# Kernel optimization log

Hardware: AMD Instinct MI355X
Metric: run time of the kernel (lower is better)

The kernel has to match this reference:

```python
import jax, jax.numpy as jnp
import numpy as np

IN_DIM = 64  # channels; theta/phi -> C//8, g -> C//2


def _maxpool2x2(t):
    # t: [B, c, H, W] -> [B, c, H//2, W//2]
    B, c, H, W = t.shape
    return t.reshape(B, c, H // 2, 2, W // 2, 2).max(axis=(3, 5))


def setup_inputs() -> dict:
    key = jax.random.key(0)
    ks = jax.random.split(key, 6)
    C = IN_DIM
    x = jax.random.normal(ks[0], (16, C, 64, 64), dtype=jnp.float32)
    # 1x1 convs stored as [out, in] matrices (kernel is 1x1, no bias)
    w_theta = jax.random.normal(ks[1], (C // 8, C), dtype=jnp.float32) * (1.0 / np.sqrt(C))
    w_phi = jax.random.normal(ks[2], (C // 8, C), dtype=jnp.float32) * (1.0 / np.sqrt(C))
    w_g = jax.random.normal(ks[3], (C // 2, C), dtype=jnp.float32) * (1.0 / np.sqrt(C))
    w_o = jax.random.normal(ks[4], (C, C // 2), dtype=jnp.float32) * (1.0 / np.sqrt(C // 2))
    gamma = jax.random.normal(ks[5], (), dtype=jnp.float32)  # torch inits to 0; nonzero for testing
    return {"x": x, "w_theta": w_theta, "w_phi": w_phi, "w_g": w_g, "w_o": w_o, "gamma": gamma}


def reference(x, w_theta, w_phi, w_g, w_o, gamma):
    B, C, H, W = x.shape
    # 1x1 conv projections (pointwise channel matmuls)
    theta = jnp.einsum('oc,bchw->bohw', w_theta, x).reshape(B, C // 8, H * W)
    phi = _maxpool2x2(jnp.einsum('oc,bchw->bohw', w_phi, x)).reshape(B, C // 8, H * W // 4)
    g = _maxpool2x2(jnp.einsum('oc,bchw->bohw', w_g, x)).reshape(B, C // 2, H * W // 4)
    # attention: [B, HW, HW/4]
    beta = jax.nn.softmax(jnp.einsum('bcn,bcm->bnm', theta, phi), axis=-1)
    # aggregate values: g @ beta^T -> [B, C//2, HW]
    o = jnp.einsum('bcm,bnm->bcn', g, beta).reshape(B, C // 2, H, W)
    o = jnp.einsum('oc,bchw->bohw', w_o, o)
    return gamma * o + x
```

## Files before the change

kernel.cpp:

```cpp
#include <hip/hip_runtime.h>

typedef _Float16 half4v __attribute__((ext_vector_type(4)));
typedef _Float16 h2     __attribute__((ext_vector_type(2)));
typedef float    float4v __attribute__((ext_vector_type(4)));

#define BB 16
#define CC 64
#define NN 4096
#define MM 1024
#define LN256 5.545177444479562f

static __device__ __forceinline__ float4v mfma16(half4v a, half4v b, float4v c) {
    return __builtin_amdgcn_mfma_f32_16x16x16f16(a, b, c, 0, 0, 0);
}

__device__ __forceinline__ unsigned pk2(float a, float b) {
    union { _Float16 h[2]; unsigned u; } cv;
    cv.h[0] = (_Float16)a; cv.h[1] = (_Float16)b;
    return cv.u;
}
__device__ __forceinline__ h2 ash2(unsigned u) {
    union { unsigned u; h2 h; } c; c.u = u; return c.h;
}
__device__ __forceinline__ h2 hmax2(h2 a, h2 b) {
    h2 r;
    r.x = (a.x > b.x) ? a.x : b.x;
    r.y = (a.y > b.y) ? a.y : b.y;
    return r;
}
__device__ __forceinline__ h2 shfl_xor_h2(h2 v, int m) {
    union { h2 h; int i; } c; c.h = v; c.i = __shfl_xor(c.i, m);
    return c.h;
}

__device__ __forceinline__ int gl_off(int c, int m) {
    return (c * 2048 + m * 2) ^ (((c ^ (m >> 6)) & 15) << 3);
}

__global__ __launch_bounds__(128, 4) void proj_kernel(
    const float* __restrict__ x,
    const float* __restrict__ w_th,
    const float* __restrict__ w_ph,
    const float* __restrict__ w_g,
    _Float16* __restrict__ theta,
    _Float16* __restrict__ phi,
    _Float16* __restrict__ gT)
{
    __shared__ __align__(16) float wlds[64 * 16];
    unsigned* wl2 = (unsigned*)wlds;

    const int b   = blockIdx.y;
    const int blk = blockIdx.x;
    const int z   = blockIdx.z;
    const int t   = threadIdx.x;

    if (z == 0) {
        for (int i = t; i < 1024; i += 128) {
            int c = i >> 4, o = i & 15;
            wlds[i] = (o < 8) ? w_th[o * 64 + c] : w_ph[(o - 8) * 64 + c];
        }
    } else {
        for (int i = t; i < 1024; i += 128) {
            int c = i >> 4, o2 = i & 15;
            wl2[i] = pk2(w_g[(2 * o2) * 64 + c], w_g[(2 * o2 + 1) * 64 + c]);
        }
    }
    __syncthreads();

    const float2* x2 = (const float2*)(x + (size_t)b * CC * NN);
    const int p2 = blk * 128 + t;
    const int l = t & 63, w = t >> 6;
    const int m = (blk * 2 + w) * 32 + (l & 31);

    if (z == 0) {
        float th0[8], th1[8], ph0[8], ph1[8];
#pragma unroll
        for (int i = 0; i < 8; i++) { th0[i]=th1[i]=ph0[i]=ph1[i]=0.f; }
#pragma unroll 4
        for (int c = 0; c < 64; c++) {
            float2 xv = x2[c * (NN / 2) + p2];
            const float4* w4 = (const float4*)&wlds[c * 16];
            float4 wv[4];
#pragma unroll
            for (int j = 0; j < 4; j++) wv[j] = w4[j];
            const float* wf = (const float*)wv;
#pragma unroll
            for (int o = 0; o < 8; o++) {
                th0[o] = fmaf(wf[o], xv.x, th0[o]);
                th1[o] = fmaf(wf[o], xv.y, th1[o]);
                ph0[o] = fmaf(wf[8 + o], xv.x, ph0[o]);
                ph1[o] = fmaf(wf[8 + o], xv.y, ph1[o]);
            }
        }
        uint4* tw = (uint4*)(theta + ((size_t)b * NN + 2 * p2) * 8);
        tw[0] = make_uint4(pk2(th0[0],th0[1]), pk2(th0[2],th0[3]),
                           pk2(th0[4],th0[5]), pk2(th0[6],th0[7]));
        tw[1] = make_uint4(pk2(th1[0],th1[1]), pk2(th1[2],th1[3]),
                           pk2(th1[4],th1[5]), pk2(th1[6],th1[7]));
        float phm[8];
#pragma unroll
        for (int i = 0; i < 8; i++) phm[i] = fmaxf(ph0[i], ph1[i]);
#pragma unroll
        for (int i = 0; i < 8; i++) phm[i] = fmaxf(phm[i], __shfl_xor(phm[i], 32));
        if (l < 32) {
            uint4* pw = (uint4*)(phi + ((size_t)b * MM + m) * 8);
            pw[0] = make_uint4(pk2(phm[0],phm[1]), pk2(phm[2],phm[3]),
                               pk2(phm[4],phm[5]), pk2(phm[6],phm[7]));
        }
    } else {
        h2 ga[16], gb[16];
#pragma unroll
        for (int i = 0; i < 16; i++) { ga[i] = (h2)0; gb[i] = (h2)0; }
#pragma unroll 4
        for (int c = 0; c < 64; c++) {
            float2 xv = x2[c * (NN / 2) + p2];
            const uint4* w4 = (const uint4*)&wl2[c * 16];
            uint4 q0 = w4[0], q1 = w4[1], q2 = w4[2], q3 = w4[3];
            unsigned wv[16] = {q0.x,q0.y,q0.z,q0.w, q1.x,q1.y,q1.z,q1.w,
                               q2.x,q2.y,q2.z,q2.w, q3.x,q3.y,q3.z,q3.w};
            _Float16 hx = (_Float16)xv.x, hy = (_Float16)xv.y;
            h2 xa; xa.x = hx; xa.y = hx;
            h2 xb; xb.x = hy; xb.y = hy;
#pragma unroll
            for (int k = 0; k < 16; k++) {
                ga[k] = __builtin_elementwise_fma(ash2(wv[k]), xa, ga[k]);
                gb[k] = __builtin_elementwise_fma(ash2(wv[k]), xb, gb[k]);
            }
        }
        h2 gm[16];
#pragma unroll
        for (int k = 0; k < 16; k++) gm[k] = hmax2(ga[k], gb[k]);
#pragma unroll
        for (int k = 0; k < 16; k++) gm[k] = hmax2(gm[k], shfl_xor_h2(gm[k], 32));
        const int k0 = (l < 32) ? 0 : 8;
        _Float16* gp = gT + ((size_t)b * 32 + 2 * k0) * MM + m;
#pragma unroll
        for (int k = 0; k < 8; k++) {
            h2 v = gm[k0 + k];
            gp[(size_t)(2 * k) * MM]     = v.x;
            gp[(size_t)(2 * k + 1) * MM] = v.y;
        }
    }
}

__global__ __launch_bounds__(512, 4) void attn_kernel(
    const _Float16* __restrict__ theta,
    const _Float16* __restrict__ phi,
    const _Float16* __restrict__ gT,
    const float* __restrict__ w_o,
    const float* __restrict__ gamma_p,
    const float* __restrict__ x,
    float* __restrict__ out)
{
    __shared__ __align__(16) _Float16 phl[MM * 8];
    __shared__ __align__(16) _Float16 gl[32 * MM];

    const int b    = blockIdx.y;
    const int t    = threadIdx.x;
    const int wave = t >> 6;
    const int lane = t & 63;
    const int col  = lane & 15;
    const int q    = lane >> 4;
    const int nbase = blockIdx.x * 128 + wave * 16;

    const float4v zero4 = {0.f, 0.f, 0.f, 0.f};
    const half4v zeroh = {0, 0, 0, 0};

    const float4* ph4 = (const float4*)(phi + (size_t)b * MM * 8);
    const float4* gt4 = (const float4*)(gT + (size_t)b * 32 * MM);
    float4 pr0 = ph4[t], pr1 = ph4[t + 512];
    float4 gr[8];
#pragma unroll
    for (int j = 0; j < 8; j++) gr[j] = gt4[t + j * 512];

    half4v thB = zeroh;
    if (q < 2)
        thB = *(const half4v*)(theta + ((size_t)b * NN + nbase + col) * 8 + q * 4);

    half4v onesA = zeroh;
    if (col == 0) {
        onesA[0] = (_Float16)1; onesA[1] = (_Float16)1;
        onesA[2] = (_Float16)1; onesA[3] = (_Float16)1;
    }

    char* phb = (char*)phl;
    {
        int m = t;
        *(float2*)(phb + ((m * 16)     ^ (m & 8))) = *(const float2*)&pr0;
        *(float2*)(phb + ((m * 16 + 8) ^ (m & 8))) = *((const float2*)&pr0 + 1);
        m = t + 512;
        *(float2*)(phb + ((m * 16)     ^ (m & 8))) = *(const float2*)&pr1;
        *(float2*)(phb + ((m * 16 + 8) ^ (m & 8))) = *((const float2*)&pr1 + 1);
    }
    __syncthreads();

    float mx = -1e30f;
#pragma unroll 4
    for (int mt = 0; mt < 64; mt++) {
        half4v af = zeroh;
        if (q < 2) {
            int m = mt * 16 + col;
            af = *(const half4v*)(phb + ((m * 16 + q * 8) ^ (m & 8)));
        }
        float4v S = mfma16(af, thB, zero4);
        mx = fmaxf(mx, fmaxf(fmaxf(S.x, S.y), fmaxf(S.z, S.w)));
    }
    mx = fmaxf(mx, __shfl_xor(mx, 16));
    mx = fmaxf(mx, __shfl_xor(mx, 32));
    const float shift = mx - LN256;

    char* glb = (char*)gl;
#pragma unroll
    for (int j = 0; j < 8; j++) {
        int idx4 = t + j * 512;
        int c = idx4 >> 7;
        int m = (idx4 & 127) * 8;
        *(float2*)(glb + gl_off(c, m))     = *(const float2*)&gr[j];
        *(float2*)(glb + gl_off(c, m + 4)) = *((const float2*)&gr[j] + 1);
    }
    __syncthreads();

    float4v acc0 = zero4, acc1 = zero4, accd = zero4;
#pragma unroll 4
    for (int mt = 0; mt < 64; mt++) {
        half4v af = zeroh;
        if (q < 2) {
            int m = mt * 16 + col;
            af = *(const half4v*)(phb + ((m * 16 + q * 8) ^ (m & 8)));
        }
        float4v S = mfma16(af, thB, zero4);
        half4v P;
        P[0] = (_Float16)__expf(S.x - shift);
        P[1] = (_Float16)__expf(S.y - shift);
        P[2] = (_Float16)__expf(S.z - shift);
        P[3] = (_Float16)__expf(S.w - shift);
        const int m0 = mt * 16 + q * 4;
        half4v ag0 = *(const half4v*)(glb + gl_off(col,      m0));
        half4v ag1 = *(const half4v*)(glb + gl_off(col + 16, m0));
        acc0 = mfma16(ag0, P, acc0);
        acc1 = mfma16(ag1, P, acc1);
        accd = mfma16(onesA, P, accd);
    }

    float dv = __shfl(accd.x, col);
    float sc = gamma_p[0] / dv;

    half4v B0, B1;
    B0[0] = (_Float16)(acc0.x * sc); B0[1] = (_Float16)(acc0.y * sc);
    B0[2] = (_Float16)(acc0.z * sc); B0[3] = (_Float16)(acc0.w * sc);
    B1[0] = (_Float16)(acc1.x * sc); B1[1] = (_Float16)(acc1.y * sc);
    B1[2] = (_Float16)(acc1.z * sc); B1[3] = (_Float16)(acc1.w * sc);

#pragma unroll
    for (int ct = 0; ct < 4; ct++) {
        const float* wp = w_o + (size_t)(ct * 16 + col) * 32 + q * 4;
        float4 w0 = *(const float4*)wp;
        float4 w1 = *(const float4*)(wp + 16);
        half4v wa, wb;
        wa[0] = (_Float16)w0.x; wa[1] = (_Float16)w0.y;
        wa[2] = (_Float16)w0.z; wa[3] = (_Float16)w0.w;
        wb[0] = (_Float16)w1.x; wb[1] = (_Float16)w1.y;
        wb[2] = (_Float16)w1.z; wb[3] = (_Float16)w1.w;
        float4v D = mfma16(wa, B0, zero4);
        D = mfma16(wb, B1, D);
#pragma unroll
        for (int r = 0; r < 4; r++) {
            int co = ct * 16 + q * 4 + r;
            size_t idx = ((size_t)b * CC + co) * NN + nbase + col;
            out[idx] = D[r] + x[idx];
        }
    }
}

extern "C" void kernel_launch(void* const* d_in, const int* in_sizes, int n_in,
                              void* d_out, int out_size, void* d_ws, size_t ws_size,
                              hipStream_t stream) {
    const float* x       = (const float*)d_in[0];
    const float* w_theta = (const float*)d_in[1];
    const float* w_phi   = (const float*)d_in[2];
    const float* w_g     = (const float*)d_in[3];
    const float* w_o     = (const float*)d_in[4];
    const float* gamma   = (const float*)d_in[5];
    float* out = (float*)d_out;

    _Float16* theta_ws = (_Float16*)d_ws;
    _Float16* phi_ws   = theta_ws + (size_t)BB * NN * 8;
    _Float16* gT_ws    = phi_ws   + (size_t)BB * MM * 8;

    proj_kernel<<<dim3(16, BB, 2), 128, 0, stream>>>(
        x, w_theta, w_phi, w_g, theta_ws, phi_ws, gT_ws);

    attn_kernel<<<dim3(NN / 128, BB), 512, 0, stream>>>(
        theta_ws, phi_ws, gT_ws, w_o, gamma, x, out);
}
```

Before: 120.8 us.

## Fuse theta/phi and g projections into one pass and prefetch residual x

The projection kernel no longer splits theta/phi and g work across a z-dimension. Each thread now loads x once per channel and computes all three projections, with pixel mapping changed to spatial 2x2 pooling via lane shuffles (xor 1 and xor 32). This halves x reads in the projection stage at the cost of higher register pressure per thread. Separately, the attention kernel loads the residual x values into registers before the main loop, so their latency overlaps the compute.

```diff
diff --git a/kernel.cpp b/kernel.cpp
--- a/kernel.cpp
+++ b/kernel.cpp
@@ -37,7 +37,7 @@
     return (c * 2048 + m * 2) ^ (((c ^ (m >> 6)) & 15) << 3);
 }
 
-__global__ __launch_bounds__(128, 4) void proj_kernel(
+__global__ __launch_bounds__(256, 2) void proj_kernel(
     const float* __restrict__ x,
     const float* __restrict__ w_th,
     const float* __restrict__ w_ph,
@@ -46,92 +46,82 @@
     _Float16* __restrict__ phi,
     _Float16* __restrict__ gT)
 {
-    __shared__ __align__(16) float wlds[64 * 16];
-    unsigned* wl2 = (unsigned*)wlds;
+    __shared__ __align__(16) float    wlds[64 * 16];
+    __shared__ __align__(16) unsigned wl2[64 * 16];
 
     const int b   = blockIdx.y;
     const int blk = blockIdx.x;
-    const int z   = blockIdx.z;
     const int t   = threadIdx.x;
 
-    if (z == 0) {
-        for (int i = t; i < 1024; i += 128) {
-            int c = i >> 4, o = i & 15;
-            wlds[i] = (o < 8) ? w_th[o * 64 + c] : w_ph[(o - 8) * 64 + c];
-        }
-    } else {
-        for (int i = t; i < 1024; i += 128) {
-            int c = i >> 4, o2 = i & 15;
-            wl2[i] = pk2(w_g[(2 * o2) * 64 + c], w_g[(2 * o2 + 1) * 64 + c]);
-        }
+    for (int i = t; i < 1024; i += 256) {
+        int c = i >> 4, o = i & 15;
+        wlds[i] = (o < 8) ? w_th[o * 64 + c] : w_ph[(o - 8) * 64 + c];
+        wl2[i]  = pk2(w_g[(2 * o) * 64 + c], w_g[(2 * o + 1) * 64 + c]);
     }
     __syncthreads();
 
-    const float2* x2 = (const float2*)(x + (size_t)b * CC * NN);
-    const int p2 = blk * 128 + t;
-    const int l = t & 63, w = t >> 6;
-    const int m = (blk * 2 + w) * 32 + (l & 31);
-
-    if (z == 0) {
-        float th0[8], th1[8], ph0[8], ph1[8];
-#pragma unroll
-        for (int i = 0; i < 8; i++) { th0[i]=th1[i]=ph0[i]=ph1[i]=0.f; }
+    const int w = t >> 6, l = t & 63;
+    const int tile = blk * 4 + w;
+    const int rp   = tile >> 1;
+    const int ch   = tile & 1;
+    const int y    = rp * 2 + (l >> 5);
+    const int xcol = ch * 32 + (l & 31);
+    const int n    = y * 64 + xcol;
+    const float* xb = x + (size_t)b * CC * NN + n;
+
+    float th[8], ph[8];
+    h2 ga[16];
+#pragma unroll
+    for (int i = 0; i < 8; i++) { th[i] = 0.f; ph[i] = 0.f; }
+#pragma unroll
+    for (int i = 0; i < 16; i++) ga[i] = (h2)0;
+
 #pragma unroll 4
-        for (int c = 0; c < 64; c++) {
-            float2 xv = x2[c * (NN / 2) + p2];
-            const float4* w4 = (const float4*)&wlds[c * 16];
-            float4 wv[4];
-#pragma unroll
-            for (int j = 0; j < 4; j++) wv[j] = w4[j];
-            const float* wf = (const float*)wv;
-#pragma unroll
-            for (int o = 0; o < 8; o++) {
-                th0[o] = fmaf(wf[o], xv.x, th0[o]);
-                th1[o] = fmaf(wf[o], xv.y, th1[o]);
-                ph0[o] = fmaf(wf[8 + o], xv.x, ph0[o]);
-                ph1[o] = fmaf(wf[8 + o], xv.y, ph1[o]);
-            }
-        }
-        uint4* tw = (uint4*)(theta + ((size_t)b * NN + 2 * p2) * 8);
-        tw[0] = make_uint4(pk2(th0[0],th0[1]), pk2(th0[2],th0[3]),
-                           pk2(th0[4],th0[5]), pk2(th0[6],th0[7]));
-        tw[1] = make_uint4(pk2(th1[0],th1[1]), pk2(th1[2],th1[3]),
-                           pk2(th1[4],th1[5]), pk2(th1[6],th1[7]));
-        float phm[8];
-#pragma unroll
-        for (int i = 0; i < 8; i++) phm[i] = fmaxf(ph0[i], ph1[i]);
-#pragma unroll
-        for (int i = 0; i < 8; i++) phm[i] = fmaxf(phm[i], __shfl_xor(phm[i], 32));
+    for (int c = 0; c < 64; c++) {
+        float xv = xb[(size_t)c * NN];
+        const float4* w4 = (const float4*)&wlds[c * 16];
+        float4 wv[4];
+#pragma unroll
+        for (int j = 0; j < 4; j++) wv[j] = w4[j];
+        const float* wf = (const float*)wv;
+#pragma unroll
+        for (int o = 0; o < 8; o++) {
+            th[o] = fmaf(wf[o], xv, th[o]);
+            ph[o] = fmaf(wf[8 + o], xv, ph[o]);
+        }
+        const uint4* g4 = (const uint4*)&wl2[c * 16];
+        uint4 q0 = g4[0], q1 = g4[1], q2 = g4[2], q3 = g4[3];
+        unsigned gv[16] = {q0.x,q0.y,q0.z,q0.w, q1.x,q1.y,q1.z,q1.w,
+                           q2.x,q2.y,q2.z,q2.w, q3.x,q3.y,q3.z,q3.w};
+        _Float16 hx = (_Float16)xv;
+        h2 xa; xa.x = hx; xa.y = hx;
+#pragma unroll
+        for (int k = 0; k < 16; k++)
+            ga[k] = __builtin_elementwise_fma(ash2(gv[k]), xa, ga[k]);
+    }
+
+    uint4 tv = make_uint4(pk2(th[0],th[1]), pk2(th[2],th[3]),
+                          pk2(th[4],th[5]), pk2(th[6],th[7]));
+    *(uint4*)(theta + ((size_t)b * NN + n) * 8) = tv;
+
+    float phm[8];
+#pragma unroll
+    for (int i = 0; i < 8; i++) phm[i] = fmaxf(ph[i], __shfl_xor(ph[i], 1));
+#pragma unroll
+    for (int i = 0; i < 8; i++) phm[i] = fmaxf(phm[i], __shfl_xor(phm[i], 32));
+    h2 gm[16];
+#pragma unroll
+    for (int k = 0; k < 16; k++) gm[k] = hmax2(ga[k], shfl_xor_h2(ga[k], 1));
+#pragma unroll
+    for (int k = 0; k < 16; k++) gm[k] = hmax2(gm[k], shfl_xor_h2(gm[k], 32));
+
+    if ((l & 1) == 0) {
+        const int m = rp * 32 + ch * 16 + ((l & 31) >> 1);
         if (l < 32) {
-            uint4* pw = (uint4*)(phi + ((size_t)b * MM + m) * 8);
-            pw[0] = make_uint4(pk2(phm[0],phm[1]), pk2(phm[2],phm[3]),
-                               pk2(phm[4],phm[5]), pk2(phm[6],phm[7]));
-        }
-    } else {
-        h2 ga[16], gb[16];
-#pragma unroll
-        for (int i = 0; i < 16; i++) { ga[i] = (h2)0; gb[i] = (h2)0; }
-#pragma unroll 4
-        for (int c = 0; c < 64; c++) {
-            float2 xv = x2[c * (NN / 2) + p2];
-            const uint4* w4 = (const uint4*)&wl2[c * 16];
-            uint4 q0 = w4[0], q1 = w4[1], q2 = w4[2], q3 = w4[3];
-            unsigned wv[16] = {q0.x,q0.y,q0.z,q0.w, q1.x,q1.y,q1.z,q1.w,
-                               q2.x,q2.y,q2.z,q2.w, q3.x,q3.y,q3.z,q3.w};
-            _Float16 hx = (_Float16)xv.x, hy = (_Float16)xv.y;
-            h2 xa; xa.x = hx; xa.y = hx;
-            h2 xb; xb.x = hy; xb.y = hy;
-#pragma unroll
-            for (int k = 0; k < 16; k++) {
-                ga[k] = __builtin_elementwise_fma(ash2(wv[k]), xa, ga[k]);
-                gb[k] = __builtin_elementwise_fma(ash2(wv[k]), xb, gb[k]);
-            }
-        }
-        h2 gm[16];
-#pragma unroll
-        for (int k = 0; k < 16; k++) gm[k] = hmax2(ga[k], gb[k]);
-#pragma unroll
-        for (int k = 0; k < 16; k++) gm[k] = hmax2(gm[k], shfl_xor_h2(gm[k], 32));
+            *(uint4*)(phi + ((size_t)b * MM + m) * 8) =
+                make_uint4(pk2(phm[0],phm[1]), pk2(phm[2],phm[3]),
+                           pk2(phm[4],phm[5]), pk2(phm[6],phm[7]));
+        }
         const int k0 = (l < 32) ? 0 : 8;
         _Float16* gp = gT + ((size_t)b * 32 + 2 * k0) * MM + m;
 #pragma unroll
@@ -219,6 +209,15 @@
         *(float2*)(glb + gl_off(c, m + 4)) = *((const float2*)&gr[j] + 1);
     }
     __syncthreads();
+
+    float xr[16];
+#pragma unroll
+    for (int ct = 0; ct < 4; ct++)
+#pragma unroll
+        for (int r = 0; r < 4; r++) {
+            int co = ct * 16 + q * 4 + r;
+            xr[ct * 4 + r] = x[((size_t)b * CC + co) * NN + nbase + col];
+        }
 
     float4v acc0 = zero4, acc1 = zero4, accd = zero4;
 #pragma unroll 4
@@ -267,7 +266,7 @@
         for (int r = 0; r < 4; r++) {
             int co = ct * 16 + q * 4 + r;
             size_t idx = ((size_t)b * CC + co) * NN + nbase + col;
-            out[idx] = D[r] + x[idx];
+            out[idx] = D[r] + xr[ct * 4 + r];
         }
     }
 }
@@ -287,7 +286,7 @@
     _Float16* phi_ws   = theta_ws + (size_t)BB * NN * 8;
     _Float16* gT_ws    = phi_ws   + (size_t)BB * MM * 8;
 
-    proj_kernel<<<dim3(16, BB, 2), 128, 0, stream>>>(
+    proj_kernel<<<dim3(16, BB), 256, 0, stream>>>(
         x, w_theta, w_phi, w_g, theta_ws, phi_ws, gT_ws);
 
     attn_kernel<<<dim3(NN / 128, BB), 512, 0, stream>>>(
```

Result: slower. 127.2 us (+5.3%).
